# Performance work log

Hardware: AMD Instinct MI355X
Metric: run time of the kernel (lower is better)

## Reference

```python
import jax, jax.numpy as jnp
import numpy as np

NUM_DIRECTIONS = 64
NUM_STEPS = 64
D = 64
NEG_INF = -1e9  # matches the original's -inf sentinel of 1e9


def _sample_directions(n):
    # Mirrors WeightedEulerCurve._obtainDirection with np.random.seed(4)
    np.random.seed(4)
    out = []
    for _ in range(n):
        phi = np.random.uniform(0, np.pi * 2)
        costheta = np.random.uniform(-1, 1)
        theta = np.arccos(costheta)
        out.append([np.sin(theta) * np.cos(phi), np.sin(theta) * np.sin(phi), np.cos(theta)])
    return np.asarray(out, dtype=np.float32)


def setup_inputs() -> dict:
    key = jax.random.key(0)
    # strictly positive -> dense cubical complex (every voxel is a vertex,
    # every adjacent pair an edge, etc.), matching torch.nonzero on x>0
    x = jax.random.uniform(key, (D, D, D), dtype=jnp.float32) + 1e-3
    dirs = jnp.asarray(_sample_directions(NUM_DIRECTIONS))  # (K, 3)
    return {"x": x, "dirs": dirs}


def _pairmax(a, axis):
    n = a.shape[axis]
    return jnp.maximum(jax.lax.slice_in_dim(a, 0, n - 1, axis=axis),
                       jax.lax.slice_in_dim(a, 1, n, axis=axis))


def _curve_contrib(heights, vals, intervals):
    # heights: (K, N) per-direction simplex heights; vals: (N,) shared weights
    K = heights.shape[0]
    idx = jnp.argsort(heights, axis=-1)
    sorted_h = jnp.take_along_axis(heights, idx, axis=-1)
    sorted_v = jnp.take(vals, idx)                                    # (K, N)
    csum = jnp.concatenate([jnp.zeros((K, 1), heights.dtype),
                            jnp.cumsum(sorted_v, axis=-1)], axis=-1)  # (K, N+1)
    padded_h = jnp.concatenate([jnp.full((K, 1), NEG_INF, heights.dtype),
                                sorted_h], axis=-1)                   # (K, N+1)
    ptr = jax.vmap(lambda h: jnp.searchsorted(h, intervals, side='right'))(padded_h) - 1
    return jnp.take_along_axis(csum, ptr, axis=-1)                    # (K, num_intervals)


def _wect(x, dirs, num_steps):
    d = x.shape[0]
    K = dirs.shape[0]
    r = jnp.arange(d, dtype=x.dtype)
    d0, d1, d2 = dirs[:, 0], dirs[:, 1], dirs[:, 2]
    # vertex heights per direction: H[k,i,j,l] = d0*i + d1*j + d2*l
    H = (d0[:, None, None, None] * r[:, None, None]
         + d1[:, None, None, None] * r[None, :, None]
         + d2[:, None, None, None] * r[None, None, :])
    p0, p1, p2 = (jax.nn.relu(d0)[:, None], jax.nn.relu(d1)[:, None], jax.nn.relu(d2)[:, None])

    min_h = -(3.0 ** 0.5) * d
    dh = (-2.0 * min_h) / num_steps
    intervals = jnp.asarray(min_h + dh * np.arange(num_steps + 1), dtype=x.dtype)

    # vertices
    vh = H.reshape(K, -1)
    vv = x.reshape(-1)

    # edges along each axis: max over the 2 endpoints -> base height + relu(d_axis)
    eh = jnp.concatenate([
        H[:, :-1].reshape(K, -1) + p0,
        H[:, :, :-1].reshape(K, -1) + p1,
        H[:, :, :, :-1].reshape(K, -1) + p2], axis=1)
    ev = jnp.concatenate([
        _pairmax(x, 0).reshape(-1),
        _pairmax(x, 1).reshape(-1),
        _pairmax(x, 2).reshape(-1)])

    # squares spanning axis pairs (1,2), (0,2), (0,1): max over 4 corners
    sh = jnp.concatenate([
        H[:, :, :-1, :-1].reshape(K, -1) + p1 + p2,
        H[:, :-1, :, :-1].reshape(K, -1) + p0 + p2,
        H[:, :-1, :-1, :].reshape(K, -1) + p0 + p1], axis=1)
    sv = jnp.concatenate([
        _pairmax(_pairmax(x, 1), 2).reshape(-1),
        _pairmax(_pairmax(x, 0), 2).reshape(-1),
        _pairmax(_pairmax(x, 0), 1).reshape(-1)])

    # cubes: max over 8 corners
    ch = H[:, :-1, :-1, :-1].reshape(K, -1) + p0 + p1 + p2
    cv = _pairmax(_pairmax(_pairmax(x, 0), 1), 2).reshape(-1)

    v = _curve_contrib(vh, vv, intervals)
    e = _curve_contrib(eh, ev, intervals)
    s = _curve_contrib(sh, sv, intervals)
    c = _curve_contrib(ch, cv, intervals)
    return v - e + s - c  # (K, num_steps + 1)


def reference(x, dirs):
    return _wect(x, dirs, NUM_STEPS)
```

## Files before the change

### kernel.cpp

```cpp
#include <hip/hip_runtime.h>
#include <math.h>

#define NDIRS 64
#define NBIN 65
#define HSTRIDE 65
#define HIST1 4164
#define STAGEF 512
#define THREADS 256
#define WPB 4
#define SPW 2
#define NBLK 512
#define ROWF (NDIRS*NBIN)
#define MROWS 64

static constexpr float INV = 0.28867513459481287f;

__global__ __launch_bounds__(THREADS) void wect_hist(
    const float* __restrict__ x, const float* __restrict__ dirs,
    float* __restrict__ accum) {
  __shared__ float hist[WPB * HIST1];
  __shared__ float stage[WPB * STAGEF];
  const int tid = threadIdx.x;
  const int lane = tid & 63;
  const int wid  = tid >> 6;

  float4* h4 = (float4*)hist;
  for (int idx = tid; idx < WPB * HIST1 / 4; idx += THREADS)
    h4[idx] = make_float4(0.f, 0.f, 0.f, 0.f);
  __syncthreads();

  const float D0 = dirs[3*lane+0] * INV;
  const float D1 = dirs[3*lane+1] * INV;
  const float D2 = dirs[3*lane+2] * INV;
  const float Q1 = fmaxf(D0, 0.f);
  const float Q2 = fmaxf(D1, 0.f);
  const float Q3 = fmaxf(D2, 0.f);
  const float Q4 = Q2 + Q3;
  const float Q5 = Q1 + Q3;
  const float Q6 = Q1 + Q2;
  const float Q7 = Q1 + Q2 + Q3;

  float* __restrict__ myrow = hist + wid * HIST1 + lane * HSTRIDE;
  float4* __restrict__ mystage = (float4*)(stage + wid * STAGEF);

  for (int s = 0; s < SPW; ++s) {
    const int strip = (blockIdx.x * WPB + wid) * SPW + s;
    const int i = strip >> 6, j = strip & 63;
    const int l = lane;
    const float* p = x + (strip << 6) + l;
    const int dL = (l < 63) ? 1 : 0;
    const int dJ = (j < 63) ? 64 : 0;
    const int dI = (i < 63) ? 4096 : 0;
    const bool iv = dI != 0, jv = dJ != 0, lv = dL != 0;

    const float x000 = p[0],       x001 = p[dL];
    const float x010 = p[dJ],      x011 = p[dJ+dL];
    const float x100 = p[dI],      x101 = p[dI+dL];
    const float x110 = p[dI+dJ],   x111 = p[dI+dJ+dL];

    const float e0m = fmaxf(x000, x100);
    const float e1m = fmaxf(x000, x010);
    const float e2m = fmaxf(x000, x001);
    const float s12 = fmaxf(fmaxf(e1m, x001), x011);
    const float s02 = fmaxf(fmaxf(e0m, x001), x101);
    const float s01 = fmaxf(fmaxf(e0m, x010), x110);
    const float cc  = fmaxf(fmaxf(s01, fmaxf(x001, x101)), fmaxf(x011, x111));

    const float v1 = iv ? -e0m : 0.f;
    const float v2 = jv ? -e1m : 0.f;
    const float v3 = lv ? -e2m : 0.f;
    const float v4 = (jv && lv) ? s12 : 0.f;
    const float v5 = (iv && lv) ? s02 : 0.f;
    const float v6 = (iv && jv) ? s01 : 0.f;
    const float v7 = (iv && jv && lv) ? -cc : 0.f;
    const float T  = x000 + v1+v2+v3+v4+v5+v6+v7;

    mystage[2*lane]     = make_float4(T,  v1, v2, v3);
    mystage[2*lane + 1] = make_float4(v4, v5, v6, v7);

    const float u0 = (float)i * D0 + (float)j * D1;

    #pragma unroll 8
    for (int t = 0; t < 64; ++t) {
      const float4 A = mystage[2*t];
      const float4 B = mystage[2*t + 1];
      const float u  = fmaf((float)t, D2, u0);
      const float bf = ceilf(u);
      const float fr = bf - u;
      const int   ib = (int)bf + 32;
      float S = 0.f;
      S += (Q1 > fr) ? A.y : 0.f;
      S += (Q2 > fr) ? A.z : 0.f;
      S += (Q3 > fr) ? A.w : 0.f;
      S += (Q4 > fr) ? B.x : 0.f;
      S += (Q5 > fr) ? B.y : 0.f;
      S += (Q6 > fr) ? B.z : 0.f;
      S += (Q7 > fr) ? B.w : 0.f;
      float* a = myrow + ib;
      const float r0 = a[0], r1 = a[1];
      a[0] = r0 + (A.x - S);
      a[1] = r1 + S;
    }
  }

  __syncthreads();
  float* __restrict__ obase = accum + blockIdx.x * ROWF;
  for (int z = tid; z < ROWF; z += THREADS)
    obase[z] = hist[z] + hist[HIST1 + z]
             + hist[2*HIST1 + z] + hist[3*HIST1 + z];
}

__global__ __launch_bounds__(256) void wect_reduceA(
    const float* __restrict__ accum, float* __restrict__ mid) {
  const int q = blockIdx.x * 256 + threadIdx.x;
  if (q >= MROWS * ROWF) return;
  const int g = q / ROWF, z = q - g * ROWF;
  float v = 0.f;
  #pragma unroll
  for (int m = 0; m < NBLK / MROWS; ++m)
    v += accum[(g * (NBLK / MROWS) + m) * ROWF + z];
  mid[g * ROWF + z] = v;
}

__global__ __launch_bounds__(512) void wect_scan(
    const float* __restrict__ mid, float* __restrict__ out) {
  __shared__ float red[8 * NBIN];
  __shared__ float s[NBIN];
  const int k = blockIdx.x, tid = threadIdx.x;
  for (int z = tid; z < 8 * NBIN; z += 512) {
    const int g = z / NBIN, c = z - g * NBIN;
    float v = 0.f;
    #pragma unroll
    for (int r = g; r < MROWS; r += 8) v += mid[r * ROWF + k * NBIN + c];
    red[z] = v;
  }
  __syncthreads();
  if (tid < NBIN) {
    float v = 0.f;
    #pragma unroll
    for (int gg = 0; gg < 8; ++gg) v += red[gg * NBIN + tid];
    s[tid] = v;
  }
  __syncthreads();
  for (int off = 1; off < NBIN; off <<= 1) {
    float a = 0.f;
    if (tid < NBIN && tid >= off) a = s[tid - off];
    __syncthreads();
    if (tid < NBIN && tid >= off) s[tid] += a;
    __syncthreads();
  }
  if (tid < NBIN) out[k * NBIN + tid] = s[tid];
}

extern "C" void kernel_launch(void* const* d_in, const int* in_sizes, int n_in,
                              void* d_out, int out_size, void* d_ws, size_t ws_size,
                              hipStream_t stream) {
  const float* x = (const float*)d_in[0];
  const float* dirs = (const float*)d_in[1];
  float* out = (float*)d_out;
  float* accum = (float*)d_ws;
  float* mid = accum + NBLK * ROWF;

  wect_hist<<<NBLK, THREADS, 0, stream>>>(x, dirs, accum);
  wect_reduceA<<<(MROWS * ROWF + 255) / 256, 256, 0, stream>>>(accum, mid);
  wect_scan<<<NDIRS, 512, 0, stream>>>(mid, out);
}
```

Baseline: 83.53 us.

## Broadcast strip values via readlane and accumulate histogram bins in registers

Drops the LDS staging buffer and broadcasts each lane's per-voxel values with readlane instead of reading them back from shared memory. It also keeps running sums for the two active histogram bins in registers and writes to LDS only when the bin index changes, which cuts LDS read-modify-write traffic. The row stride moves to 66 to keep the final reduction indexing consistent. The cost is eight scalar readlanes per iteration and divergent flush branches, and the flush logic relies on bins moving monotonically with the sign of D2.

```diff
diff --git a/kernel.cpp b/kernel.cpp
--- a/kernel.cpp
+++ b/kernel.cpp
@@ -3,9 +3,8 @@
 
 #define NDIRS 64
 #define NBIN 65
-#define HSTRIDE 65
-#define HIST1 4164
-#define STAGEF 512
+#define HSTRIDE 66
+#define HIST1 (NDIRS*HSTRIDE)
 #define THREADS 256
 #define WPB 4
 #define SPW 2
@@ -15,11 +14,14 @@
 
 static constexpr float INV = 0.28867513459481287f;
 
+__device__ __forceinline__ float rdlane(float v, int t) {
+  return __int_as_float(__builtin_amdgcn_readlane(__float_as_int(v), t));
+}
+
 __global__ __launch_bounds__(THREADS) void wect_hist(
     const float* __restrict__ x, const float* __restrict__ dirs,
     float* __restrict__ accum) {
   __shared__ float hist[WPB * HIST1];
-  __shared__ float stage[WPB * STAGEF];
   const int tid = threadIdx.x;
   const int lane = tid & 63;
   const int wid  = tid >> 6;
@@ -39,9 +41,9 @@
   const float Q5 = Q1 + Q3;
   const float Q6 = Q1 + Q2;
   const float Q7 = Q1 + Q2 + Q3;
+  const bool pos = (D2 > 0.f);
 
   float* __restrict__ myrow = hist + wid * HIST1 + lane * HSTRIDE;
-  float4* __restrict__ mystage = (float4*)(stage + wid * STAGEF);
 
   for (int s = 0; s < SPW; ++s) {
     const int strip = (blockIdx.x * WPB + wid) * SPW + s;
@@ -75,39 +77,59 @@
     const float v7 = (iv && jv && lv) ? -cc : 0.f;
     const float T  = x000 + v1+v2+v3+v4+v5+v6+v7;
 
-    mystage[2*lane]     = make_float4(T,  v1, v2, v3);
-    mystage[2*lane + 1] = make_float4(v4, v5, v6, v7);
+    const float u0 = (float)i * D0 + (float)j * D1;
 
-    const float u0 = (float)i * D0 + (float)j * D1;
+    int   pib  = (int)ceilf(u0) + 32;
+    float acc0 = 0.f, acc1 = 0.f;
 
     #pragma unroll 8
     for (int t = 0; t < 64; ++t) {
-      const float4 A = mystage[2*t];
-      const float4 B = mystage[2*t + 1];
+      const float bT = rdlane(T,  t);
+      const float b1 = rdlane(v1, t);
+      const float b2 = rdlane(v2, t);
+      const float b3 = rdlane(v3, t);
+      const float b4 = rdlane(v4, t);
+      const float b5 = rdlane(v5, t);
+      const float b6 = rdlane(v6, t);
+      const float b7 = rdlane(v7, t);
       const float u  = fmaf((float)t, D2, u0);
       const float bf = ceilf(u);
       const float fr = bf - u;
       const int   ib = (int)bf + 32;
       float S = 0.f;
-      S += (Q1 > fr) ? A.y : 0.f;
-      S += (Q2 > fr) ? A.z : 0.f;
-      S += (Q3 > fr) ? A.w : 0.f;
-      S += (Q4 > fr) ? B.x : 0.f;
-      S += (Q5 > fr) ? B.y : 0.f;
-      S += (Q6 > fr) ? B.z : 0.f;
-      S += (Q7 > fr) ? B.w : 0.f;
-      float* a = myrow + ib;
-      const float r0 = a[0], r1 = a[1];
-      a[0] = r0 + (A.x - S);
-      a[1] = r1 + S;
+      S += (Q1 > fr) ? b1 : 0.f;
+      S += (Q2 > fr) ? b2 : 0.f;
+      S += (Q3 > fr) ? b3 : 0.f;
+      S += (Q4 > fr) ? b4 : 0.f;
+      S += (Q5 > fr) ? b5 : 0.f;
+      S += (Q6 > fr) ? b6 : 0.f;
+      S += (Q7 > fr) ? b7 : 0.f;
+
+      if (ib != pib) {
+        const int   fb = pos ? pib  : (pib + 1);
+        const float fv = pos ? acc0 : acc1;
+        myrow[fb] += fv;
+        const float c0 = pos ? acc1 : 0.f;
+        const float c1 = pos ? 0.f  : acc0;
+        acc0 = c0;
+        acc1 = c1;
+      }
+      acc0 += bT - S;
+      acc1 += S;
+      pib = ib;
     }
+    myrow[pib]     += acc0;
+    myrow[pib + 1] += acc1;
   }
 
   __syncthreads();
   float* __restrict__ obase = accum + blockIdx.x * ROWF;
-  for (int z = tid; z < ROWF; z += THREADS)
-    obase[z] = hist[z] + hist[HIST1 + z]
-             + hist[2*HIST1 + z] + hist[3*HIST1 + z];
+  for (int z = tid; z < ROWF; z += THREADS) {
+    const int r = z / NBIN, c = z - r * NBIN;
+    const int li = r * HSTRIDE + c;
+    obase[z] = hist[li] + hist[HIST1 + li]
+             + hist[2*HIST1 + li] + hist[3*HIST1 + li];
+  }
 }
 
 __global__ __launch_bounds__(256) void wect_reduceA(
```

Measured after the change: 93.31 us. 11.7% more time.

## Fuse partial-histogram reduction into hist kernel via atomic adds

Applied to the files above, without the earlier changes.

The separate reduction kernel is removed. Each histogram block now sums its four per-wave histograms with float4 LDS reads and atomically adds the result into one of 64 shared rows, after a memset zeroes those rows. This avoids writing and re-reading a large per-block partial buffer and saves one kernel launch. In exchange it adds a memset call, contention from eight blocks sharing each row, and a nondeterministic floating-point summation order.

```diff
diff --git a/kernel.cpp b/kernel.cpp
--- a/kernel.cpp
+++ b/kernel.cpp
@@ -17,7 +17,7 @@
 
 __global__ __launch_bounds__(THREADS) void wect_hist(
     const float* __restrict__ x, const float* __restrict__ dirs,
-    float* __restrict__ accum) {
+    float* __restrict__ mid) {
   __shared__ float hist[WPB * HIST1];
   __shared__ float stage[WPB * STAGEF];
   const int tid = threadIdx.x;
@@ -104,22 +104,17 @@
   }
 
   __syncthreads();
-  float* __restrict__ obase = accum + blockIdx.x * ROWF;
-  for (int z = tid; z < ROWF; z += THREADS)
-    obase[z] = hist[z] + hist[HIST1 + z]
-             + hist[2*HIST1 + z] + hist[3*HIST1 + z];
-}
-
-__global__ __launch_bounds__(256) void wect_reduceA(
-    const float* __restrict__ accum, float* __restrict__ mid) {
-  const int q = blockIdx.x * 256 + threadIdx.x;
-  if (q >= MROWS * ROWF) return;
-  const int g = q / ROWF, z = q - g * ROWF;
-  float v = 0.f;
-  #pragma unroll
-  for (int m = 0; m < NBLK / MROWS; ++m)
-    v += accum[(g * (NBLK / MROWS) + m) * ROWF + z];
-  mid[g * ROWF + z] = v;
+  float* __restrict__ mrow = mid + (blockIdx.x & (MROWS - 1)) * ROWF;
+  for (int q = tid; q < ROWF / 4; q += THREADS) {
+    const float4 a = *(const float4*)&hist[4 * q];
+    const float4 b = *(const float4*)&hist[HIST1 + 4 * q];
+    const float4 c = *(const float4*)&hist[2 * HIST1 + 4 * q];
+    const float4 d = *(const float4*)&hist[3 * HIST1 + 4 * q];
+    unsafeAtomicAdd(&mrow[4 * q + 0], a.x + b.x + c.x + d.x);
+    unsafeAtomicAdd(&mrow[4 * q + 1], a.y + b.y + c.y + d.y);
+    unsafeAtomicAdd(&mrow[4 * q + 2], a.z + b.z + c.z + d.z);
+    unsafeAtomicAdd(&mrow[4 * q + 3], a.w + b.w + c.w + d.w);
+  }
 }
 
 __global__ __launch_bounds__(512) void wect_scan(
@@ -158,10 +153,9 @@
   const float* x = (const float*)d_in[0];
   const float* dirs = (const float*)d_in[1];
   float* out = (float*)d_out;
-  float* accum = (float*)d_ws;
-  float* mid = accum + NBLK * ROWF;
+  float* mid = (float*)d_ws;
 
-  wect_hist<<<NBLK, THREADS, 0, stream>>>(x, dirs, accum);
-  wect_reduceA<<<(MROWS * ROWF + 255) / 256, 256, 0, stream>>>(accum, mid);
+  hipMemsetAsync(mid, 0, MROWS * ROWF * sizeof(float), stream);
+  wect_hist<<<NBLK, THREADS, 0, stream>>>(x, dirs, mid);
   wect_scan<<<NDIRS, 512, 0, stream>>>(mid, out);
 }
```

After: 104.1 us. 1.25x slower.
